# Kernel optimization log

Measured on AMD Instinct MI355X. Metric: run time of the kernel, lower is better.

## Reference

```python
import jax, jax.numpy as jnp
import numpy as np

B, D, DEPTH, C = 8192, 2048, 10, 1000
NUM_INNER = 2 ** DEPTH - 1   # 1023
NUM_LEAVES = 2 ** DEPTH      # 1024


def setup_inputs() -> dict:
    key = jax.random.key(0)
    k1, k2, k3, k4 = jax.random.split(key, 4)
    x = jax.random.normal(k1, (B, D), dtype=jnp.float32)
    # scale weights like a typical init so sigmoid isn't fully saturated
    W = jax.random.normal(k2, (D, NUM_INNER), dtype=jnp.float32) * 0.02
    b = jax.random.normal(k3, (NUM_INNER,), dtype=jnp.float32) * 0.02
    leaf_dist = jax.random.normal(k4, (NUM_LEAVES, C), dtype=jnp.float32)
    return {"x": x, "W": W, "b": b, "leaf_dist": leaf_dist}


def reference(x, W, b, leaf_dist):
    # inner node routing probabilities: [B, num_inner]
    decisions = jax.nn.sigmoid(x @ W + b)
    depth = int(np.log2(decisions.shape[1] + 1))
    pp = jnp.ones((x.shape[0], 1), dtype=x.dtype)  # path probs, starts at root
    for d in range(depth):  # small fixed loop over tree depth
        s, e = 2 ** d - 1, 2 ** (d + 1) - 1
        ld = decisions[:, s:e]                      # [B, 2^d]
        pp = jnp.concatenate([pp * ld, pp * (1.0 - ld)], axis=1)  # [B, 2^(d+1)]
        # faithful reproduction of the original's even/odd reordering
        pp = jnp.concatenate([pp[:, ::2], pp[:, 1::2]], axis=1)
    leaf_probs = jax.nn.softmax(leaf_dist, axis=1)  # [num_leaves, C]
    return pp @ leaf_probs                          # [B, C]
```

## Files before the change

kernel.cpp:

```cpp
#include <hip/hip_runtime.h>

typedef __attribute__((ext_vector_type(8))) unsigned short ushort8v;
typedef __attribute__((ext_vector_type(8))) __bf16 bf16x8;
typedef __attribute__((ext_vector_type(4))) float floatx4;

__device__ __forceinline__ unsigned short f2b(float f) {
    unsigned u = __float_as_uint(f);
    unsigned r = u + 0x7fffu + ((u >> 16) & 1u);
    return (unsigned short)(r >> 16);
}
__device__ __forceinline__ float b2f(unsigned short h) {
    return __uint_as_float(((unsigned)h) << 16);
}


__global__ __launch_bounds__(256) void prep_kernel(const float* __restrict__ x,
                                                   unsigned short* __restrict__ A2x,
                                                   const float* __restrict__ W,
                                                   unsigned short* __restrict__ B2w,
                                                   const float* __restrict__ ld_,
                                                   unsigned short* __restrict__ B2p) {
    __shared__ float tile[32 * 33];
    __shared__ float buf[1000];
    __shared__ float red[8];
    const int b = blockIdx.x, t = threadIdx.x;
    if (b < 512) {
        const int mt = b;
        const int wave = t >> 6, kco = (t >> 4) & 3, l16 = t & 15;
        const float* xr0 = x + (size_t)(mt * 16 + l16) * 2048;
#pragma unroll 4
        for (int i = 0; i < 16; i++) {
            const int kc = wave * 64 + i * 4 + kco;
            const float* xr = xr0 + kc * 8;
            float4 v0 = *(const float4*)xr;
            float4 v1 = *(const float4*)(xr + 4);
            ushort8v o;
            o[0] = f2b(v0.x); o[1] = f2b(v0.y); o[2] = f2b(v0.z); o[3] = f2b(v0.w);
            o[4] = f2b(v1.x); o[5] = f2b(v1.y); o[6] = f2b(v1.z); o[7] = f2b(v1.w);
            *(ushort8v*)(A2x + ((size_t)(mt * 256 + kc) * 16 + l16) * 8) = o;
        }
    } else if (b < 2560) {
        const int idx = b - 512;
        const int n0 = (idx & 31) * 32, k0 = (idx >> 5) * 32;
        const int tx = t & 31, ty = t >> 5;
#pragma unroll
        for (int i = 0; i < 4; i++) {
            int k = k0 + ty + i * 8, n = n0 + tx;
            tile[(ty + i * 8) * 33 + tx] = (n < 1023) ? W[(size_t)k * 1023 + n] : 0.f;
        }
        __syncthreads();
#pragma unroll
        for (int i = 0; i < 4; i++) {
            int n = n0 + ty + i * 8, k = k0 + tx;
            size_t off = ((size_t)((n >> 4) * 256 + (k >> 3)) * 16 + (n & 15)) * 8 + (k & 7);
            B2w[off] = f2b(tile[tx * 33 + ty + i * 8]);
        }
    } else {
        const int l0 = b - 2560;
        const float* r = ld_ + (size_t)l0 * 1000;
        float mx = -3.4e38f;
        for (int i = t; i < 1000; i += 256) { float v = r[i]; buf[i] = v; mx = fmaxf(mx, v); }
#pragma unroll
        for (int o = 32; o > 0; o >>= 1) mx = fmaxf(mx, __shfl_down(mx, o));
        if ((t & 63) == 0) red[t >> 6] = mx;
        __syncthreads();
        mx = fmaxf(fmaxf(red[0], red[1]), fmaxf(red[2], red[3]));
        float s = 0.f;
        for (int i = t; i < 1000; i += 256) { float e = __expf(buf[i] - mx); buf[i] = e; s += e; }
#pragma unroll
        for (int o = 32; o > 0; o >>= 1) s += __shfl_down(s, o);
        if ((t & 63) == 0) red[4 + (t >> 6)] = s;
        __syncthreads();
        float inv = 1.f / (red[4] + red[5] + red[6] + red[7]);
        for (int i = t; i < 1024; i += 256) {
            float pv = (i < 1000) ? buf[i] * inv : 0.f;
            size_t off = ((size_t)((i >> 4) * 128 + (l0 >> 3)) * 16 + (i & 15)) * 8 + (l0 & 7);
            B2p[off] = f2b(pv);
        }
    }
}

__global__ __launch_bounds__(256) void pp_kernel(const unsigned short* __restrict__ dec,
                                                 unsigned short* __restrict__ A2p) {
    __shared__ float d[1024];
    __shared__ float pa[1024], pb[1024];
    const int t = threadIdx.x;
    const int rrow = blockIdx.x;
    const unsigned short* row = dec + (size_t)rrow * 1024;
    for (int i = t; i < 1024; i += 256) d[i] = (i < 1023) ? b2f(row[i]) : 0.f;
    if (t == 0) pa[0] = 1.f;
    __syncthreads();
    float* cur = pa; float* nxt = pb;
    for (int dep = 0; dep < 10; dep++) {
        const int half = 1 << dep;
        const int len = half << 1;
        for (int j = t; j < len; j += 256) {
            int tt = j >> dep;
            int s  = j & (half - 1);
            int i2 = 2 * s + tt;
            int u  = i2 >> dep;
            int rr = i2 & (half - 1);
            float dv = d[half - 1 + rr];
            nxt[j] = cur[rr] * (u ? (1.f - dv) : dv);
        }
        __syncthreads();
        float* tmp = cur; cur = nxt; nxt = tmp;
    }
    const int mtb = (rrow >> 4) * 128;
    const int li  = (rrow & 15) * 8;
    for (int i = t; i < 1024; i += 256) {
        size_t off = ((size_t)(mtb + (i >> 3)) * 16) * 8 + li + (i & 7);
        A2p[off] = f2b(cur[i]);
    }
}

template <int EPI>
__global__ __launch_bounds__(128, 1) void gemm_frag(const unsigned short* __restrict__ A2,
                                                    const unsigned short* __restrict__ B2,
                                                    const float* __restrict__ bias,
                                                    unsigned short* __restrict__ obf,
                                                    float* __restrict__ of32,
                                                    int KC, int ldo) {
    const int tid  = threadIdx.x;
    const int lane = tid & 63;
    const int wave = tid >> 6;
    const int quad = lane >> 4, l16 = lane & 15;

    const int l   = blockIdx.x;
    const int xcd = l & 7;
    const int j   = l >> 3;
    const int bm  = xcd * 8 + (j & 7);
    const int bn  = j >> 3;

    const int mt0 = bm * 8 + wave * 4;
    const int nt0 = bn * 8;

    const int lofs = (quad * 16 + l16) * 8;
    const unsigned short* ap[4];
    const unsigned short* bp[8];
#pragma unroll
    for (int mi = 0; mi < 4; mi++) ap[mi] = A2 + (size_t)(mt0 + mi) * KC * 128 + lofs;
#pragma unroll
    for (int ni = 0; ni < 8; ni++) bp[ni] = B2 + (size_t)(nt0 + ni) * KC * 128 + lofs;

    floatx4 acc[4][8] = {};
    const int NIT = KC >> 2;

#pragma unroll 2
    for (int it = 0; it < NIT; it++) {
        const size_t ko = (size_t)it * 512;
        bf16x8 af[4], bfv[8];
#pragma unroll
        for (int mi = 0; mi < 4; mi++)
            af[mi] = __builtin_bit_cast(bf16x8, *(const ushort8v*)(ap[mi] + ko));
#pragma unroll
        for (int ni = 0; ni < 8; ni++)
            bfv[ni] = __builtin_bit_cast(bf16x8, *(const ushort8v*)(bp[ni] + ko));
#pragma unroll
        for (int mi = 0; mi < 4; mi++)
#pragma unroll
            for (int ni = 0; ni < 8; ni++)
                acc[mi][ni] = __builtin_amdgcn_mfma_f32_16x16x32_bf16(
                    af[mi], bfv[ni], acc[mi][ni], 0, 0, 0);
    }

#pragma unroll
    for (int ni = 0; ni < 8; ni++) {
        const int col = (nt0 + ni) * 16 + l16;
        float bb = 0.f;
        if constexpr (EPI == 0) bb = (col < 1023) ? bias[col] : 0.f;
#pragma unroll
        for (int mi = 0; mi < 4; mi++) {
            const int row0 = (mt0 + mi) * 16 + quad * 4;
#pragma unroll
            for (int r = 0; r < 4; r++) {
                float v = acc[mi][ni][r];
                if constexpr (EPI == 0) {
                    float sgm = 1.f / (1.f + __expf(-(v + bb)));
                    obf[(size_t)(row0 + r) * ldo + col] = f2b(sgm);
                } else {
                    if (col < 1000) of32[(size_t)(row0 + r) * ldo + col] = v;
                }
            }
        }
    }
}

extern "C" void kernel_launch(void* const* d_in, const int* in_sizes, int n_in,
                              void* d_out, int out_size, void* d_ws, size_t ws_size,
                              hipStream_t stream) {
    const float* x   = (const float*)d_in[0];
    const float* W   = (const float*)d_in[1];
    const float* b   = (const float*)d_in[2];
    const float* ldd = (const float*)d_in[3];
    float* out = (float*)d_out;

    char* ws = (char*)d_ws;
    unsigned short* A2x = (unsigned short*)(ws);
    unsigned short* A2p = (unsigned short*)(ws);
    unsigned short* B2w = (unsigned short*)(ws + 33554432);
    unsigned short* dec = (unsigned short*)(ws + 37748736);
    unsigned short* B2p = (unsigned short*)(ws + 54525952);

    prep_kernel<<<3584, 256, 0, stream>>>(x, A2x, W, B2w, ldd, B2p);
    gemm_frag<0><<<512, 128, 0, stream>>>(A2x, B2w, b, dec, nullptr, 256, 1024);
    pp_kernel<<<8192, 256, 0, stream>>>(dec, A2p);
    gemm_frag<1><<<512, 128, 0, stream>>>(A2p, B2p, nullptr, nullptr, out, 128, 1000);
}
```

Baseline: 228.5 us.

## Batch eight rows per pp block, split x conversion, double-buffer GEMM fragment loads

The path-probability kernel now handles eight rows per block with vectorized decision loads, so the early tree depths with few active threads waste less of the block. The x-to-bf16 conversion is split across four times more blocks. The GEMM loop explicitly double-buffers its A/B fragment registers and asks for two blocks per CU. Costs are higher LDS use in pp_kernel and more register pressure in the GEMM, which may cause spills.

Result: faster. 214.3 us (-6.2%).

```diff
diff --git a/kernel.cpp b/kernel.cpp
--- a/kernel.cpp
+++ b/kernel.cpp
@@ -24,13 +24,13 @@
     __shared__ float buf[1000];
     __shared__ float red[8];
     const int b = blockIdx.x, t = threadIdx.x;
-    if (b < 512) {
-        const int mt = b;
-        const int wave = t >> 6, kco = (t >> 4) & 3, l16 = t & 15;
+    if (b < 2048) {
+        const int mt = b >> 2, kq = (b & 3) * 64;
+        const int kco = t >> 4, l16 = t & 15;
         const float* xr0 = x + (size_t)(mt * 16 + l16) * 2048;
-#pragma unroll 4
-        for (int i = 0; i < 16; i++) {
-            const int kc = wave * 64 + i * 4 + kco;
+#pragma unroll
+        for (int i = 0; i < 4; i++) {
+            const int kc = kq + i * 16 + kco;
             const float* xr = xr0 + kc * 8;
             float4 v0 = *(const float4*)xr;
             float4 v1 = *(const float4*)(xr + 4);
@@ -39,8 +39,8 @@
             o[4] = f2b(v1.x); o[5] = f2b(v1.y); o[6] = f2b(v1.z); o[7] = f2b(v1.w);
             *(ushort8v*)(A2x + ((size_t)(mt * 256 + kc) * 16 + l16) * 8) = o;
         }
-    } else if (b < 2560) {
-        const int idx = b - 512;
+    } else if (b < 4096) {
+        const int idx = b - 2048;
         const int n0 = (idx & 31) * 32, k0 = (idx >> 5) * 32;
         const int tx = t & 31, ty = t >> 5;
 #pragma unroll
@@ -56,7 +56,7 @@
             B2w[off] = f2b(tile[tx * 33 + ty + i * 8]);
         }
     } else {
-        const int l0 = b - 2560;
+        const int l0 = b - 4096;
         const float* r = ld_ + (size_t)l0 * 1000;
         float mx = -3.4e38f;
         for (int i = t; i < 1000; i += 256) { float v = r[i]; buf[i] = v; mx = fmaxf(mx, v); }
@@ -82,40 +82,47 @@
 
 __global__ __launch_bounds__(256) void pp_kernel(const unsigned short* __restrict__ dec,
                                                  unsigned short* __restrict__ A2p) {
-    __shared__ float d[1024];
-    __shared__ float pa[1024], pb[1024];
+    __shared__ unsigned short dsh[8 * 1024];
+    __shared__ float pa[8 * 1024];
+    __shared__ float pb[8 * 1024];
     const int t = threadIdx.x;
-    const int rrow = blockIdx.x;
-    const unsigned short* row = dec + (size_t)rrow * 1024;
-    for (int i = t; i < 1024; i += 256) d[i] = (i < 1023) ? b2f(row[i]) : 0.f;
-    if (t == 0) pa[0] = 1.f;
+    const int r0 = blockIdx.x * 8;
+    {
+        const ushort8v* src = (const ushort8v*)(dec + (size_t)r0 * 1024);
+        ushort8v* dst = (ushort8v*)dsh;
+        for (int g = t; g < 1024; g += 256) dst[g] = src[g];
+    }
+    if (t < 8) pa[t * 1024] = 1.f;
     __syncthreads();
     float* cur = pa; float* nxt = pb;
     for (int dep = 0; dep < 10; dep++) {
         const int half = 1 << dep;
-        const int len = half << 1;
-        for (int j = t; j < len; j += 256) {
+        const int len  = half << 1;
+        const int total = len << 3;
+        for (int idx = t; idx < total; idx += 256) {
+            const int r = idx >> (dep + 1);
+            const int j = idx & (len - 1);
             int tt = j >> dep;
             int s  = j & (half - 1);
             int i2 = 2 * s + tt;
             int u  = i2 >> dep;
             int rr = i2 & (half - 1);
-            float dv = d[half - 1 + rr];
-            nxt[j] = cur[rr] * (u ? (1.f - dv) : dv);
+            float dv = b2f(dsh[r * 1024 + half - 1 + rr]);
+            nxt[r * 1024 + j] = cur[r * 1024 + rr] * (u ? (1.f - dv) : dv);
         }
         __syncthreads();
         float* tmp = cur; cur = nxt; nxt = tmp;
     }
-    const int mtb = (rrow >> 4) * 128;
-    const int li  = (rrow & 15) * 8;
-    for (int i = t; i < 1024; i += 256) {
-        size_t off = ((size_t)(mtb + (i >> 3)) * 16) * 8 + li + (i & 7);
-        A2p[off] = f2b(cur[i]);
+    for (int i = t; i < 8192; i += 256) {
+        const int r = i >> 10, j = i & 1023;
+        const int rrow = r0 + r;
+        size_t off = ((size_t)((rrow >> 4) * 128 + (j >> 3)) * 16 + (rrow & 15)) * 8 + (j & 7);
+        A2p[off] = f2b(cur[r * 1024 + j]);
     }
 }
 
 template <int EPI>
-__global__ __launch_bounds__(128, 1) void gemm_frag(const unsigned short* __restrict__ A2,
+__global__ __launch_bounds__(128, 2) void gemm_frag(const unsigned short* __restrict__ A2,
                                                     const unsigned short* __restrict__ B2,
                                                     const float* __restrict__ bias,
                                                     unsigned short* __restrict__ obf,
@@ -146,22 +153,45 @@
     floatx4 acc[4][8] = {};
     const int NIT = KC >> 2;
 
-#pragma unroll 2
-    for (int it = 0; it < NIT; it++) {
-        const size_t ko = (size_t)it * 512;
-        bf16x8 af[4], bfv[8];
+    bf16x8 a0[4], b0[8], a1[4], b1[8];
+#pragma unroll
+    for (int mi = 0; mi < 4; mi++)
+        a0[mi] = __builtin_bit_cast(bf16x8, *(const ushort8v*)(ap[mi]));
+#pragma unroll
+    for (int ni = 0; ni < 8; ni++)
+        b0[ni] = __builtin_bit_cast(bf16x8, *(const ushort8v*)(bp[ni]));
+
+    for (int it = 0; it < NIT; it += 2) {
+        {
+            const size_t ko = (size_t)(it + 1) * 512;
+#pragma unroll
+            for (int mi = 0; mi < 4; mi++)
+                a1[mi] = __builtin_bit_cast(bf16x8, *(const ushort8v*)(ap[mi] + ko));
+#pragma unroll
+            for (int ni = 0; ni < 8; ni++)
+                b1[ni] = __builtin_bit_cast(bf16x8, *(const ushort8v*)(bp[ni] + ko));
+        }
 #pragma unroll
         for (int mi = 0; mi < 4; mi++)
-            af[mi] = __builtin_bit_cast(bf16x8, *(const ushort8v*)(ap[mi] + ko));
-#pragma unroll
-        for (int ni = 0; ni < 8; ni++)
-            bfv[ni] = __builtin_bit_cast(bf16x8, *(const ushort8v*)(bp[ni] + ko));
+#pragma unroll
+            for (int ni = 0; ni < 8; ni++)
+                acc[mi][ni] = __builtin_amdgcn_mfma_f32_16x16x32_bf16(
+                    a0[mi], b0[ni], acc[mi][ni], 0, 0, 0);
+        if (it + 2 < NIT) {
+            const size_t ko = (size_t)(it + 2) * 512;
+#pragma unroll
+            for (int mi = 0; mi < 4; mi++)
+                a0[mi] = __builtin_bit_cast(bf16x8, *(const ushort8v*)(ap[mi] + ko));
+#pragma unroll
+            for (int ni = 0; ni < 8; ni++)
+                b0[ni] = __builtin_bit_cast(bf16x8, *(const ushort8v*)(bp[ni] + ko));
+        }
 #pragma unroll
         for (int mi = 0; mi < 4; mi++)
 #pragma unroll
             for (int ni = 0; ni < 8; ni++)
                 acc[mi][ni] = __builtin_amdgcn_mfma_f32_16x16x32_bf16(
-                    af[mi], bfv[ni], acc[mi][ni], 0, 0, 0);
+                    a1[mi], b1[ni], acc[mi][ni], 0, 0, 0);
     }
 
 #pragma unroll
@@ -202,8 +232,8 @@
     unsigned short* dec = (unsigned short*)(ws + 37748736);
     unsigned short* B2p = (unsigned short*)(ws + 54525952);
 
-    prep_kernel<<<3584, 256, 0, stream>>>(x, A2x, W, B2w, ldd, B2p);
+    prep_kernel<<<5120, 256, 0, stream>>>(x, A2x, W, B2w, ldd, B2p);
     gemm_frag<0><<<512, 128, 0, stream>>>(A2x, B2w, b, dec, nullptr, 256, 1024);
-    pp_kernel<<<8192, 256, 0, stream>>>(dec, A2p);
+    pp_kernel<<<1024, 256, 0, stream>>>(dec, A2p);
     gemm_frag<1><<<512, 128, 0, stream>>>(A2p, B2p, nullptr, nullptr, out, 128, 1000);
 }
```
